# Kernel optimization log

Hardware: AMD Instinct MI355X
Metric: run time of the kernel (lower is better)

## Reference

```python
import jax, jax.numpy as jnp
import numpy as np

L, D = 8192, 1024


def binary_operator_diag(q_i, q_j):
    # elementwise (diagonal) linear-recurrence combine: h_j = A_j * h_i + b_j
    A_i, b_i = q_i
    A_j, b_j = q_j
    return A_j * A_i, A_j * b_i + b_j


def setup_inputs() -> dict:
    key = jax.random.key(0)
    k_in, k_u, k_th, k_bre, k_bim = jax.random.split(key, 5)
    inputs = jax.random.normal(k_in, (L, D), dtype=jnp.float32)
    # stable LRU init: |lambda| = exp(-exp(nu)) = sqrt(u), u in (0.01, 0.99)
    u = jax.random.uniform(k_u, (D,), jnp.float32, 0.01, 0.99)
    nu = jnp.log(-0.5 * jnp.log(u))
    # phase stored in log-space (forward uses exp(theta))
    theta = jnp.log(jax.random.uniform(k_th, (D,), jnp.float32, 1e-3, 6.28))
    gamma_log = 0.5 * jnp.log(1.0 - u)  # = log(sqrt(1 - |lambda|^2))
    norm = np.float32(np.sqrt(2.0 * D))
    B_re = jax.random.normal(k_bre, (D, D), jnp.float32) / norm
    B_im = jax.random.normal(k_bim, (D, D), jnp.float32) / norm
    return {"inputs": inputs, "theta": theta, "nu": nu,
            "gamma_log": gamma_log, "B_re": B_re, "B_im": B_im}


def reference(inputs, theta, nu, gamma_log, B_re, B_im):
    # diagonal transition: lambda = exp(-exp(nu) + i*exp(theta)), shape [D]
    diag_lambda = jnp.exp(-jnp.exp(nu) + 1j * jnp.exp(theta))
    # normalized input matrix: (B_re + i B_im) * exp(gamma_log)[:, None]
    B_norm = (B_re + 1j * B_im) * jnp.exp(gamma_log)[:, None]  # [D, D] complex
    # Bu[t] = B_norm @ u_t  -> batched as one GEMM: [L, D] complex
    Bu = jnp.einsum('ld,kd->lk', inputs.astype(B_norm.dtype), B_norm)
    Lambda_elements = jnp.broadcast_to(diag_lambda[None, :], Bu.shape)
    # parallel associative scan over time (axis 0), elementwise over channels
    _, hidden_states = jax.lax.associative_scan(
        binary_operator_diag, (Lambda_elements, Bu))
    return hidden_states.real + inputs
```

## Files before the change

### kernel.cpp

```cpp
#include <hip/hip_runtime.h>
#include <cstdint>
#include <cstddef>

typedef float  f32x4  __attribute__((ext_vector_type(4)));
typedef short  bf16x8 __attribute__((ext_vector_type(8)));
typedef unsigned short u16x8 __attribute__((ext_vector_type(8)));

#define L_SEQ   8192
#define D_DIM   1024
#define N_COL   2048
#define N_PAIR  512
#define CHUNK_T 16
#define N_CHUNK 512

__device__ __forceinline__ unsigned short f2bf(float f) {
  unsigned int b = __float_as_uint(f);
  b += 0x7FFFu + ((b >> 16) & 1u);
  return (unsigned short)(b >> 16);
}
__device__ __forceinline__ float bf2f(unsigned short u) {
  return __uint_as_float((unsigned int)u << 16);
}
__device__ __forceinline__ void gload_lds16(const void* g, void* lds) {
  __builtin_amdgcn_global_load_lds(
      (const __attribute__((address_space(1))) void*)g,
      (__attribute__((address_space(3))) void*)lds, 16, 0, 0);
}
__device__ __forceinline__ float2 cmul(float2 a, float2 b) {
  return make_float2(a.x * b.x - a.y * b.y, a.x * b.y + a.y * b.x);
}
__device__ __forceinline__ float2 csqr(float2 a) {
  return make_float2(a.x * a.x - a.y * a.y, 2.f * a.x * a.y);
}
__device__ __forceinline__ void cfma2(const float4& lm, float2& h0, float2& h1,
                                      const float4& v) {
  float nr0 = fmaf(lm.x, h0.x, fmaf(-lm.y, h0.y, v.x));
  float ni0 = fmaf(lm.x, h0.y, fmaf(lm.y, h0.x, v.y));
  float nr1 = fmaf(lm.z, h1.x, fmaf(-lm.w, h1.y, v.z));
  float ni1 = fmaf(lm.z, h1.y, fmaf(lm.w, h1.x, v.w));
  h0.x = nr0; h0.y = ni0; h1.x = nr1; h1.y = ni1;
}

__global__ __launch_bounds__(256) void k_prep(
    const float* __restrict__ in, const float* __restrict__ Bre,
    const float* __restrict__ Bim, const float* __restrict__ gamma_log,
    const float* __restrict__ theta, const float* __restrict__ nu,
    unsigned short* __restrict__ A, unsigned short* __restrict__ W,
    float2* __restrict__ lam) {
  int b = blockIdx.x;
  if (b < 4096) {
    int i = b * 256 + threadIdx.x;
    const float4* p = (const float4*)in;
    float4 a = p[2 * i], c = p[2 * i + 1];
    u16x8 o;
    o[0] = f2bf(a.x); o[1] = f2bf(a.y); o[2] = f2bf(a.z); o[3] = f2bf(a.w);
    o[4] = f2bf(c.x); o[5] = f2bf(c.y); o[6] = f2bf(c.z); o[7] = f2bf(c.w);
    *(u16x8*)(A + (size_t)i * 8) = o;
  } else if (b < 5120) {
    int t = (b - 4096) * 256 + threadIdx.x;
    int row = t >> 7;
    int seg = t & 127;
    int k = row >> 1;
    const float* src = (row & 1) ? Bim : Bre;
    float g = expf(gamma_log[k]);
    const float4* p = (const float4*)(src + (size_t)k * D_DIM + seg * 8);
    float4 a = p[0], c = p[1];
    u16x8 o;
    o[0] = f2bf(a.x * g); o[1] = f2bf(a.y * g); o[2] = f2bf(a.z * g); o[3] = f2bf(a.w * g);
    o[4] = f2bf(c.x * g); o[5] = f2bf(c.y * g); o[6] = f2bf(c.z * g); o[7] = f2bf(c.w * g);
    *(u16x8*)(W + (size_t)row * D_DIM + seg * 8) = o;
  } else {
    int k = (b - 5120) * 256 + threadIdx.x;
    if (k < D_DIM) {
      float mod = expf(-expf(nu[k]));
      float ang = expf(theta[k]);
      lam[k] = make_float2(mod * cosf(ang), mod * sinf(ang));
    }
  }
}

__global__ __launch_bounds__(512, 1) void k_gemm(const unsigned short* __restrict__ A,
                                                 const unsigned short* __restrict__ W,
                                                 float* __restrict__ Bu) {
  extern __shared__ char smem[];

  const int tid = threadIdx.x;
  const int l = tid & 63, w = tid >> 6;
  const int wm = w >> 2, wn = w & 3;

  int orig = blockIdx.x;
  int wgid = (orig & 7) * 32 + (orig >> 3);
  const int mt = wgid >> 3, nt = wgid & 7;
  const size_t m0 = (size_t)mt * 256, n0 = (size_t)nt * 256;

  const int srow = tid >> 3;
  const int scs  = tid & 7;
  const int cA   = scs ^ (srow & 7);
  const size_t srcoff0 = (size_t)srow * 2048 + (size_t)cA * 16;
  const size_t srcoff1 = srcoff0 + 64 * 2048;
  const int dst0 = tid * 16, dst1 = 8192 + tid * 16;

#define STAGE(Mptr, Mbase, Msel, bb, hh, TT) do {                                   \
    const char* s_ = (const char*)(Mptr) +                                          \
        (((Mbase) + (size_t)(hh) * 128) * 2048 + (size_t)(TT) * 128);               \
    char* d_ = smem + (Msel) * 65536 + (bb) * 32768 + (hh) * 16384;                 \
    gload_lds16(s_ + srcoff0, d_ + dst0);                                           \
    gload_lds16(s_ + srcoff1, d_ + dst1);                                           \
  } while (0)

  int aroff[8], broff[4];
#pragma unroll
  for (int fr = 0; fr < 8; ++fr) {
    int lrow = fr * 32 + wm * 16 + (l & 15);
    aroff[fr] = (lrow >> 7) * 16384 + (lrow & 127) * 128;
  }
#pragma unroll
  for (int fn = 0; fn < 4; ++fn) {
    int lrow = fn * 64 + wn * 16 + (l & 15);
    broff[fn] = (lrow >> 7) * 16384 + (lrow & 127) * 128;
  }
  const int swk0 = (((l >> 4)) ^ (l & 7)) << 4;
  const int swk1 = ((4 + (l >> 4)) ^ (l & 7)) << 4;

  f32x4 acc[8][4];
#pragma unroll
  for (int m = 0; m < 8; ++m)
#pragma unroll
    for (int n = 0; n < 4; ++n) acc[m][n] = (f32x4){0.f, 0.f, 0.f, 0.f};

  bf16x8 af[4][2], bfr[4][2];

#define LGKMC0 asm volatile("s_waitcnt lgkmcnt(0)" ::: "memory")
#define VMCNT4 asm volatile("s_waitcnt vmcnt(4)" ::: "memory")
#define BAR()  do { asm volatile("" ::: "memory"); __builtin_amdgcn_s_barrier(); \
                    asm volatile("" ::: "memory"); } while (0)

  STAGE(W, n0, 1, 0, 0, 0);
  STAGE(A, m0, 0, 0, 1, 0);
  STAGE(A, m0, 0, 0, 0, 0);
  STAGE(W, n0, 1, 0, 1, 0);
  STAGE(W, n0, 1, 1, 0, 1);
  STAGE(A, m0, 0, 1, 1, 1);
  VMCNT4;
  BAR();

  for (int kt = 0; kt < 16; ++kt) {
    const int buf = kt & 1;
    const int abase = buf * 32768;
    const int bbase = 65536 + buf * 32768;
    const int t1 = (kt + 1 < 16) ? kt + 1 : 15;
    const int t2 = (kt + 2 < 16) ? kt + 2 : 15;
    const int b1 = (kt + 1) & 1, b2 = kt & 1;

#pragma unroll
    for (int i = 0; i < 4; ++i) {
      af[i][0] = *(const bf16x8*)(smem + abase + aroff[i] + swk0);
      af[i][1] = *(const bf16x8*)(smem + abase + aroff[i] + swk1);
    }
#pragma unroll
    for (int fn = 0; fn < 2; ++fn) {
      bfr[fn][0] = *(const bf16x8*)(smem + bbase + broff[fn] + swk0);
      bfr[fn][1] = *(const bf16x8*)(smem + bbase + broff[fn] + swk1);
    }
    STAGE(A, m0, 0, b1, 0, t1);
    __builtin_amdgcn_s_setprio(1);
#pragma unroll
    for (int i = 0; i < 4; ++i)
#pragma unroll
      for (int fn = 0; fn < 2; ++fn) {
        acc[i][fn] = __builtin_amdgcn_mfma_f32_16x16x32_bf16(af[i][0], bfr[fn][0], acc[i][fn], 0, 0, 0);
        acc[i][fn] = __builtin_amdgcn_mfma_f32_16x16x32_bf16(af[i][1], bfr[fn][1], acc[i][fn], 0, 0, 0);
      }
    __builtin_amdgcn_s_setprio(0);
    LGKMC0;
    BAR();

#pragma unroll
    for (int fn = 2; fn < 4; ++fn) {
      bfr[fn][0] = *(const bf16x8*)(smem + bbase + broff[fn] + swk0);
      bfr[fn][1] = *(const bf16x8*)(smem + bbase + broff[fn] + swk1);
    }
    STAGE(W, n0, 1, b1, 1, t1);
    __builtin_amdgcn_s_setprio(1);
#pragma unroll
    for (int i = 0; i < 4; ++i)
#pragma unroll
      for (int fn = 2; fn < 4; ++fn) {
        acc[i][fn] = __builtin_amdgcn_mfma_f32_16x16x32_bf16(af[i][0], bfr[fn][0], acc[i][fn], 0, 0, 0);
        acc[i][fn] = __builtin_amdgcn_mfma_f32_16x16x32_bf16(af[i][1], bfr[fn][1], acc[i][fn], 0, 0, 0);
      }
    __builtin_amdgcn_s_setprio(0);
    LGKMC0;
    BAR();

#pragma unroll
    for (int i = 0; i < 4; ++i) {
      af[i][0] = *(const bf16x8*)(smem + abase + aroff[4 + i] + swk0);
      af[i][1] = *(const bf16x8*)(smem + abase + aroff[4 + i] + swk1);
    }
    STAGE(W, n0, 1, b2, 0, t2);
    __builtin_amdgcn_s_setprio(1);
#pragma unroll
    for (int i = 0; i < 4; ++i)
#pragma unroll
      for (int fn = 2; fn < 4; ++fn) {
        acc[4 + i][fn] = __builtin_amdgcn_mfma_f32_16x16x32_bf16(af[i][0], bfr[fn][0], acc[4 + i][fn], 0, 0, 0);
        acc[4 + i][fn] = __builtin_amdgcn_mfma_f32_16x16x32_bf16(af[i][1], bfr[fn][1], acc[4 + i][fn], 0, 0, 0);
      }
    __builtin_amdgcn_s_setprio(0);
    LGKMC0;
    BAR();

    STAGE(A, m0, 0, b2, 1, t2);
    __builtin_amdgcn_s_setprio(1);
#pragma unroll
    for (int i = 0; i < 4; ++i)
#pragma unroll
      for (int fn = 0; fn < 2; ++fn) {
        acc[4 + i][fn] = __builtin_amdgcn_mfma_f32_16x16x32_bf16(af[i][0], bfr[fn][0], acc[4 + i][fn], 0, 0, 0);
        acc[4 + i][fn] = __builtin_amdgcn_mfma_f32_16x16x32_bf16(af[i][1], bfr[fn][1], acc[4 + i][fn], 0, 0, 0);
      }
    __builtin_amdgcn_s_setprio(0);
    VMCNT4;
    BAR();
  }
#undef STAGE

#pragma unroll
  for (int fr = 0; fr < 8; ++fr)
#pragma unroll
    for (int fn = 0; fn < 4; ++fn) {
      size_t col = n0 + fn * 64 + wn * 16 + (l & 15);
#pragma unroll
      for (int j = 0; j < 4; ++j) {
        size_t row = m0 + fr * 32 + wm * 16 + (l >> 4) * 4 + j;
        Bu[row * N_COL + col] = acc[fr][fn][j];
      }
    }
}

__global__ __launch_bounds__(256) void k_scan1(const float4* __restrict__ Bu4,
                                               const float4* __restrict__ lam4,
                                               float4* __restrict__ agg4) {
  int t = blockIdx.x * 256 + threadIdx.x;
  int c = t >> 9, j = t & 511;
  float4 lm = lam4[j];
  float2 h0 = {0.f, 0.f}, h1 = {0.f, 0.f};
  const float4* p = Bu4 + (size_t)c * CHUNK_T * N_PAIR + j;
#pragma unroll
  for (int s = 0; s < CHUNK_T; ++s) {
    float4 v = p[(size_t)s * N_PAIR];
    cfma2(lm, h0, h1, v);
  }
  agg4[(size_t)c * N_PAIR + j] = make_float4(h0.x, h0.y, h1.x, h1.y);
}

__global__ __launch_bounds__(256) void k_scan2(const float4* __restrict__ agg4,
                                               const float4* __restrict__ lam4,
                                               float4* __restrict__ carry4) {
  int wave = blockIdx.x * 4 + (threadIdx.x >> 6);
  int lane = threadIdx.x & 63;
  int j = wave;
  float4 lm = lam4[j];
  float2 lT0 = {lm.x, lm.y}, lT1 = {lm.z, lm.w};
#pragma unroll
  for (int i = 0; i < 4; ++i) { lT0 = csqr(lT0); lT1 = csqr(lT1); }

  float4 a[8];
  float2 T0 = {0.f, 0.f}, T1 = {0.f, 0.f};
  float4 lTv = make_float4(lT0.x, lT0.y, lT1.x, lT1.y);
#pragma unroll
  for (int i = 0; i < 8; ++i) {
    a[i] = agg4[(size_t)(lane * 8 + i) * N_PAIR + j];
    cfma2(lTv, T0, T1, a[i]);
  }

  float2 M0 = lT0, M1 = lT1;
#pragma unroll
  for (int i = 0; i < 3; ++i) { M0 = csqr(M0); M1 = csqr(M1); }
  float2 S0 = T0, S1 = T1;
#pragma unroll
  for (int d = 1; d < 64; d <<= 1) {
    float2 u0, u1;
    u0.x = __shfl_up(S0.x, d); u0.y = __shfl_up(S0.y, d);
    u1.x = __shfl_up(S1.x, d); u1.y = __shfl_up(S1.y, d);
    if (lane >= d) {
      float2 m0 = cmul(M0, u0), m1 = cmul(M1, u1);
      S0.x += m0.x; S0.y += m0.y; S1.x += m1.x; S1.y += m1.y;
    }
    M0 = csqr(M0); M1 = csqr(M1);
  }
  float2 P0, P1;
  P0.x = __shfl_up(S0.x, 1); P0.y = __shfl_up(S0.y, 1);
  P1.x = __shfl_up(S1.x, 1); P1.y = __shfl_up(S1.y, 1);
  if (lane == 0) { P0 = make_float2(0.f, 0.f); P1 = make_float2(0.f, 0.f); }

#pragma unroll
  for (int i = 0; i < 8; ++i) {
    carry4[(size_t)(lane * 8 + i) * N_PAIR + j] = make_float4(P0.x, P0.y, P1.x, P1.y);
    cfma2(lTv, P0, P1, a[i]);
  }
}

__global__ __launch_bounds__(256) void k_scan3(const float4* __restrict__ Bu4,
                                               const float4* __restrict__ lam4,
                                               const float4* __restrict__ carry4,
                                               const ushort4* __restrict__ inA,
                                               float4* __restrict__ out4) {
  int t = blockIdx.x * 256 + threadIdx.x;
  int c = t >> 8, q = t & 255;
  float4 lm0 = lam4[2 * q], lm1 = lam4[2 * q + 1];
  float4 cv0 = carry4[(size_t)c * N_PAIR + 2 * q];
  float4 cv1 = carry4[(size_t)c * N_PAIR + 2 * q + 1];
  float2 h0 = {cv0.x, cv0.y}, h1 = {cv0.z, cv0.w};
  float2 h2 = {cv1.x, cv1.y}, h3 = {cv1.z, cv1.w};
#pragma unroll
  for (int s = 0; s < CHUNK_T; ++s) {
    size_t row = (size_t)c * CHUNK_T + s;
    float4 v0 = Bu4[row * N_PAIR + 2 * q];
    float4 v1 = Bu4[row * N_PAIR + 2 * q + 1];
    cfma2(lm0, h0, h1, v0);
    cfma2(lm1, h2, h3, v1);
    ushort4 iv = inA[row * 256 + q];
    out4[row * 256 + q] = make_float4(h0.x + bf2f(iv.x), h1.x + bf2f(iv.y),
                                      h2.x + bf2f(iv.z), h3.x + bf2f(iv.w));
  }
}

extern "C" void kernel_launch(void* const* d_in, const int* in_sizes, int n_in,
                              void* d_out, int out_size, void* d_ws, size_t ws_size,
                              hipStream_t stream) {
  (void)in_sizes; (void)n_in; (void)out_size; (void)ws_size;
  const float* inputs    = (const float*)d_in[0];
  const float* theta     = (const float*)d_in[1];
  const float* nu        = (const float*)d_in[2];
  const float* gamma_log = (const float*)d_in[3];
  const float* Bre       = (const float*)d_in[4];
  const float* Bim       = (const float*)d_in[5];

  char* ws = (char*)d_ws;
  float2*         lam   = (float2*)ws;
  unsigned short* A     = (unsigned short*)(ws + (1 << 16));
  unsigned short* W     = (unsigned short*)(ws + (1 << 16) + (16u << 20));
  float*          Bu    = (float*)(ws + (1 << 16) + (20u << 20));
  float4*         agg   = (float4*)(ws + (1 << 16) + (84u << 20));
  float4*         carry = (float4*)(ws + (1 << 16) + (88u << 20));

  static_assert(sizeof(float4) == 16, "");
  hipFuncSetAttribute((const void*)k_gemm,
                      hipFuncAttributeMaxDynamicSharedMemorySize, 131072);

  k_prep<<<5124, 256, 0, stream>>>(inputs, Bre, Bim, gamma_log, theta, nu, A, W, lam);
  k_gemm<<<256, 512, 131072, stream>>>(A, W, Bu);
  k_scan1<<<(N_CHUNK * N_PAIR) / 256, 256, 0, stream>>>((const float4*)Bu,
                                                        (const float4*)lam, agg);
  k_scan2<<<N_PAIR / 4, 256, 0, stream>>>(agg, (const float4*)lam, carry);
  k_scan3<<<(N_CHUNK * 256) / 256, 256, 0, stream>>>((const float4*)Bu,
                                                     (const float4*)lam, carry,
                                                     (const ushort4*)A,
                                                     (float4*)d_out);
}
```

Baseline: 86.82 us.

## Fuse chunk-aggregate scan into GEMM epilogue and store Bu as bf16

After: 69.59 us. 1.25x faster.

```diff
diff --git a/kernel.cpp b/kernel.cpp
--- a/kernel.cpp
+++ b/kernel.cpp
@@ -81,7 +81,9 @@
 
 __global__ __launch_bounds__(512, 1) void k_gemm(const unsigned short* __restrict__ A,
                                                  const unsigned short* __restrict__ W,
-                                                 float* __restrict__ Bu) {
+                                                 unsigned short* __restrict__ Bu16,
+                                                 float2* __restrict__ agg2,
+                                                 const float2* __restrict__ lam) {
   extern __shared__ char smem[];
 
   const int tid = threadIdx.x;
@@ -132,6 +134,7 @@
 
 #define LGKMC0 asm volatile("s_waitcnt lgkmcnt(0)" ::: "memory")
 #define VMCNT4 asm volatile("s_waitcnt vmcnt(4)" ::: "memory")
+#define VMCNT0 asm volatile("s_waitcnt vmcnt(0)" ::: "memory")
 #define BAR()  do { asm volatile("" ::: "memory"); __builtin_amdgcn_s_barrier(); \
                     asm volatile("" ::: "memory"); } while (0)
 
@@ -148,9 +151,8 @@
     const int buf = kt & 1;
     const int abase = buf * 32768;
     const int bbase = 65536 + buf * 32768;
-    const int t1 = (kt + 1 < 16) ? kt + 1 : 15;
-    const int t2 = (kt + 2 < 16) ? kt + 2 : 15;
     const int b1 = (kt + 1) & 1, b2 = kt & 1;
+    const bool s1 = (kt + 1 < 16), s2 = (kt + 2 < 16);
 
 #pragma unroll
     for (int i = 0; i < 4; ++i) {
@@ -162,7 +164,7 @@
       bfr[fn][0] = *(const bf16x8*)(smem + bbase + broff[fn] + swk0);
       bfr[fn][1] = *(const bf16x8*)(smem + bbase + broff[fn] + swk1);
     }
-    STAGE(A, m0, 0, b1, 0, t1);
+    if (s1) STAGE(A, m0, 0, b1, 0, kt + 1);
     __builtin_amdgcn_s_setprio(1);
 #pragma unroll
     for (int i = 0; i < 4; ++i)
@@ -180,7 +182,7 @@
       bfr[fn][0] = *(const bf16x8*)(smem + bbase + broff[fn] + swk0);
       bfr[fn][1] = *(const bf16x8*)(smem + bbase + broff[fn] + swk1);
     }
-    STAGE(W, n0, 1, b1, 1, t1);
+    if (s1) STAGE(W, n0, 1, b1, 1, kt + 1);
     __builtin_amdgcn_s_setprio(1);
 #pragma unroll
     for (int i = 0; i < 4; ++i)
@@ -198,7 +200,7 @@
       af[i][0] = *(const bf16x8*)(smem + abase + aroff[4 + i] + swk0);
       af[i][1] = *(const bf16x8*)(smem + abase + aroff[4 + i] + swk1);
     }
-    STAGE(W, n0, 1, b2, 0, t2);
+    if (s2) STAGE(W, n0, 1, b2, 0, kt + 2);
     __builtin_amdgcn_s_setprio(1);
 #pragma unroll
     for (int i = 0; i < 4; ++i)
@@ -211,7 +213,7 @@
     LGKMC0;
     BAR();
 
-    STAGE(A, m0, 0, b2, 1, t2);
+    if (s2) STAGE(A, m0, 0, b2, 1, kt + 2);
     __builtin_amdgcn_s_setprio(1);
 #pragma unroll
     for (int i = 0; i < 4; ++i)
@@ -221,7 +223,7 @@
         acc[4 + i][fn] = __builtin_amdgcn_mfma_f32_16x16x32_bf16(af[i][1], bfr[fn][1], acc[4 + i][fn], 0, 0, 0);
       }
     __builtin_amdgcn_s_setprio(0);
-    VMCNT4;
+    if (kt < 14) VMCNT4; else VMCNT0;
     BAR();
   }
 #undef STAGE
@@ -230,29 +232,47 @@
   for (int fr = 0; fr < 8; ++fr)
 #pragma unroll
     for (int fn = 0; fn < 4; ++fn) {
-      size_t col = n0 + fn * 64 + wn * 16 + (l & 15);
+      int col = fn * 64 + wn * 16 + (l & 15);
 #pragma unroll
       for (int j = 0; j < 4; ++j) {
-        size_t row = m0 + fr * 32 + wm * 16 + (l >> 4) * 4 + j;
-        Bu[row * N_COL + col] = acc[fr][fn][j];
-      }
-    }
-}
-
-__global__ __launch_bounds__(256) void k_scan1(const float4* __restrict__ Bu4,
-                                               const float4* __restrict__ lam4,
-                                               float4* __restrict__ agg4) {
-  int t = blockIdx.x * 256 + threadIdx.x;
-  int c = t >> 9, j = t & 511;
-  float4 lm = lam4[j];
-  float2 h0 = {0.f, 0.f}, h1 = {0.f, 0.f};
-  const float4* p = Bu4 + (size_t)c * CHUNK_T * N_PAIR + j;
-#pragma unroll
-  for (int s = 0; s < CHUNK_T; ++s) {
-    float4 v = p[(size_t)s * N_PAIR];
-    cfma2(lm, h0, h1, v);
-  }
-  agg4[(size_t)c * N_PAIR + j] = make_float4(h0.x, h0.y, h1.x, h1.y);
+        int row = fr * 32 + wm * 16 + (l >> 4) * 4 + j;
+        int byte = row * 512 + ((col * 2) ^ ((row & 7) << 4));
+        *(unsigned short*)(smem + byte) = f2bf(acc[fr][fn][j]);
+      }
+    }
+  __syncthreads();
+
+  {
+    unsigned short* gbase = Bu16 + m0 * N_COL + n0;
+#pragma unroll
+    for (int pass = 0; pass < 16; ++pass) {
+      int row = pass * 16 + (tid >> 5);
+      int c = tid & 31;
+      int byte = row * 512 + ((c * 16) ^ ((row & 7) << 4));
+      f32x4 v = *(const f32x4*)(smem + byte);
+      *(f32x4*)(gbase + (size_t)row * N_COL + c * 8) = v;
+    }
+  }
+
+#pragma unroll
+  for (int i = 0; i < 4; ++i) {
+    int q = i * 512 + tid;
+    int c = q >> 7, ch = q & 127;
+    float2 lmv = lam[(n0 >> 1) + ch];
+    float2 h = {0.f, 0.f};
+#pragma unroll
+    for (int s = 0; s < 16; ++s) {
+      int row = c * 16 + s;
+      int byte = row * 512 + ((ch * 4) ^ ((row & 7) << 4));
+      unsigned int pr = *(const unsigned int*)(smem + byte);
+      float br = bf2f((unsigned short)(pr & 0xFFFFu));
+      float bi = bf2f((unsigned short)(pr >> 16));
+      float nr = fmaf(lmv.x, h.x, fmaf(-lmv.y, h.y, br));
+      float ni = fmaf(lmv.x, h.y, fmaf(lmv.y, h.x, bi));
+      h.x = nr; h.y = ni;
+    }
+    agg2[(size_t)(mt * 16 + c) * 1024 + (n0 >> 1) + ch] = h;
+  }
 }
 
 __global__ __launch_bounds__(256) void k_scan2(const float4* __restrict__ agg4,
@@ -302,7 +322,7 @@
   }
 }
 
-__global__ __launch_bounds__(256) void k_scan3(const float4* __restrict__ Bu4,
+__global__ __launch_bounds__(256) void k_scan3(const u16x8* __restrict__ Bu8,
                                                const float4* __restrict__ lam4,
                                                const float4* __restrict__ carry4,
                                                const ushort4* __restrict__ inA,
@@ -317,8 +337,9 @@
 #pragma unroll
   for (int s = 0; s < CHUNK_T; ++s) {
     size_t row = (size_t)c * CHUNK_T + s;
-    float4 v0 = Bu4[row * N_PAIR + 2 * q];
-    float4 v1 = Bu4[row * N_PAIR + 2 * q + 1];
+    u16x8 b = Bu8[row * 256 + q];
+    float4 v0 = make_float4(bf2f(b[0]), bf2f(b[1]), bf2f(b[2]), bf2f(b[3]));
+    float4 v1 = make_float4(bf2f(b[4]), bf2f(b[5]), bf2f(b[6]), bf2f(b[7]));
     cfma2(lm0, h0, h1, v0);
     cfma2(lm1, h2, h3, v1);
     ushort4 iv = inA[row * 256 + q];
@@ -342,20 +363,17 @@
   float2*         lam   = (float2*)ws;
   unsigned short* A     = (unsigned short*)(ws + (1 << 16));
   unsigned short* W     = (unsigned short*)(ws + (1 << 16) + (16u << 20));
-  float*          Bu    = (float*)(ws + (1 << 16) + (20u << 20));
-  float4*         agg   = (float4*)(ws + (1 << 16) + (84u << 20));
-  float4*         carry = (float4*)(ws + (1 << 16) + (88u << 20));
-
-  static_assert(sizeof(float4) == 16, "");
+  unsigned short* Bu16  = (unsigned short*)(ws + (1 << 16) + (20u << 20));
+  float2*         agg   = (float2*)(ws + (1 << 16) + (52u << 20));
+  float4*         carry = (float4*)(ws + (1 << 16) + (56u << 20));
+
   hipFuncSetAttribute((const void*)k_gemm,
                       hipFuncAttributeMaxDynamicSharedMemorySize, 131072);
 
   k_prep<<<5124, 256, 0, stream>>>(inputs, Bre, Bim, gamma_log, theta, nu, A, W, lam);
-  k_gemm<<<256, 512, 131072, stream>>>(A, W, Bu);
-  k_scan1<<<(N_CHUNK * N_PAIR) / 256, 256, 0, stream>>>((const float4*)Bu,
-                                                        (const float4*)lam, agg);
-  k_scan2<<<N_PAIR / 4, 256, 0, stream>>>(agg, (const float4*)lam, carry);
-  k_scan3<<<(N_CHUNK * 256) / 256, 256, 0, stream>>>((const float4*)Bu,
+  k_gemm<<<256, 512, 131072, stream>>>(A, W, Bu16, agg, (const float2*)lam);
+  k_scan2<<<N_PAIR / 4, 256, 0, stream>>>((const float4*)agg, (const float4*)lam, carry);
+  k_scan3<<<(N_CHUNK * 256) / 256, 256, 0, stream>>>((const u16x8*)Bu16,
                                                      (const float4*)lam, carry,
                                                      (const ushort4*)A,
                                                      (float4*)d_out);
```
